# Kernel tuning notes

Hardware: AMD Instinct MI355X
Metric: run time of the kernel (lower is better)

## Reference

```python
import jax, jax.numpy as jnp
import numpy as np

EPS = 1e-12  # undefined global `eps` in the original source; standard tiny epsilon


def setup_inputs() -> dict:
    key = jax.random.key(0)
    k1, k2 = jax.random.split(key)
    B, C = 32768, 1000
    output = jax.random.normal(k1, (B, C), dtype=jnp.float32)
    multilabels = (jax.random.uniform(k2, (B, C)) < 0.05).astype(jnp.float32)
    multilabels = multilabels.at[:, 0].set(1.0)
    return {"output": output, "multilabels": multilabels}


def reference(output, multilabels):
    # Equivalent closed form of: for every nonempty subset g of true labels,
    #   loss(g) = -[ pseudo_y*log(o+eps) + (1-pseudo_y)*log(1-o+eps) ].sum()
    #           = base - sum_{j in g} gain_j,
    # with base = -sum_j log(1-o_j+eps) and gain_j = log(o_j+eps)-log(1-o_j+eps).
    # min over nonempty subsets = base - max nonempty-subset gain
    #   = base - (sum of positive gains over true labels, or the max single
    #      gain among true labels if all gains are negative).
    o = jax.nn.sigmoid(output)                      # [B, C]
    log_p = jnp.log(o + EPS)
    log_np = jnp.log(1.0 - o + EPS)
    base = -jnp.sum(log_np, axis=1)                 # [B]
    gain = log_p - log_np                           # [B, C]
    is_true = multilabels == 1.0                    # [B, C] bool (constant)
    pos = is_true & (gain > 0)
    pos_gain = jnp.sum(jnp.where(pos, gain, 0.0), axis=1)          # [B]
    any_pos = jnp.any(pos, axis=1)                                  # [B]
    best_single = jnp.max(jnp.where(is_true, gain, -jnp.inf), axis=1)  # [B]
    max_gain = jnp.where(any_pos, pos_gain, best_single)
    per_sample = base - max_gain                    # [B]
    return jnp.mean(per_sample)
```

## Files before the change

kernel.cpp:

```cpp
#include <hip/hip_runtime.h>
#include <math.h>


constexpr int B = 32768;
constexpr int C = 1000;
constexpr int BLOCKS = 2048;
constexpr int THREADS = 256;
constexpr int WAVES_PER_BLOCK = 4;

__device__ __forceinline__ void elem_update(float x, float m,
                                            float& base, float& pos, float& best) {
    float e  = __expf(-fabsf(x));
    float xp = fmaxf(x, 0.0f);
    base += xp + __logf(1.0f + e);
    pos  += m * xp;
    if (m != 0.0f) best = fmaxf(best, x);
}

__device__ __forceinline__ void vec_update(const float4& x, const float4& m,
                                           float& base, float& pos, float& best) {
    elem_update(x.x, m.x, base, pos, best);
    elem_update(x.y, m.y, base, pos, best);
    elem_update(x.z, m.z, base, pos, best);
    elem_update(x.w, m.w, base, pos, best);
}

__global__ __launch_bounds__(THREADS)
void row_loss_kernel(const float* __restrict__ X,
                     const float* __restrict__ M,
                     float* __restrict__ partial) {
    const int lane = threadIdx.x & 63;
    const int sub  = lane & 15;
    const int grp  = lane >> 4;
    const int wave_in_block = threadIdx.x >> 6;
    const int gwave = blockIdx.x * WAVES_PER_BLOCK + wave_in_block;
    const int row   = gwave * 4 + grp;

    const float4* x4 = reinterpret_cast<const float4*>(X + (size_t)row * C);
    const float4* m4 = reinterpret_cast<const float4*>(M + (size_t)row * C);

    float4 xA[4], mA[4], xB[4], mB[4];

    #pragma unroll
    for (int j = 0; j < 4; ++j) { int i = sub + 16*j;       xA[j] = x4[i]; mA[j] = m4[i]; }
    #pragma unroll
    for (int j = 0; j < 4; ++j) { int i = sub + 64 + 16*j;  xB[j] = x4[i]; mB[j] = m4[i]; }

    float base = 0.f, pos = 0.f, best = -INFINITY;

    #pragma unroll
    for (int j = 0; j < 4; ++j) vec_update(xA[j], mA[j], base, pos, best);

    #pragma unroll
    for (int j = 0; j < 4; ++j) { int i = sub + 128 + 16*j; xA[j] = x4[i]; mA[j] = m4[i]; }

    #pragma unroll
    for (int j = 0; j < 4; ++j) vec_update(xB[j], mB[j], base, pos, best);

    #pragma unroll
    for (int j = 0; j < 3; ++j) { int i = sub + 192 + 16*j; xB[j] = x4[i]; mB[j] = m4[i]; }
    if (sub < 10) { xB[3] = x4[sub + 240]; mB[3] = m4[sub + 240]; }
    else {
        xB[3] = make_float4(-1e30f, -1e30f, -1e30f, -1e30f);
        mB[3] = make_float4(0.f, 0.f, 0.f, 0.f);
    }

    #pragma unroll
    for (int j = 0; j < 4; ++j) vec_update(xA[j], mA[j], base, pos, best);
    #pragma unroll
    for (int j = 0; j < 4; ++j) vec_update(xB[j], mB[j], base, pos, best);

    #pragma unroll
    for (int off = 8; off > 0; off >>= 1) {
        base += __shfl_down(base, off, 16);
        pos  += __shfl_down(pos,  off, 16);
        best  = fmaxf(best, __shfl_down(best, off, 16));
    }

    float per = base - ((pos > 0.f) ? pos : best);
    float v = (sub == 0) ? per : 0.f;
    v += __shfl_down(v, 32, 64);
    v += __shfl_down(v, 16, 64);

    __shared__ float s[WAVES_PER_BLOCK];
    if (lane == 0) s[wave_in_block] = v;
    __syncthreads();
    if (threadIdx.x == 0) {
        float t = 0.0f;
        #pragma unroll
        for (int i = 0; i < WAVES_PER_BLOCK; ++i) t += s[i];
        partial[blockIdx.x] = t;
    }
}

__global__ __launch_bounds__(256)
void finalize_kernel(const float* __restrict__ partial, float* __restrict__ out) {
    double t = 0.0;
    for (int i = threadIdx.x; i < BLOCKS; i += 256) t += (double)partial[i];

    #pragma unroll
    for (int off = 32; off > 0; off >>= 1)
        t += __shfl_down(t, off, 64);

    __shared__ double s[4];
    const int lane = threadIdx.x & 63;
    const int w    = threadIdx.x >> 6;
    if (lane == 0) s[w] = t;
    __syncthreads();
    if (threadIdx.x == 0) {
        double r = s[0] + s[1] + s[2] + s[3];
        out[0] = (float)(r / (double)B);
    }
}

extern "C" void kernel_launch(void* const* d_in, const int* in_sizes, int n_in,
                              void* d_out, int out_size, void* d_ws, size_t ws_size,
                              hipStream_t stream) {
    const float* X  = (const float*)d_in[0];
    const float* M  = (const float*)d_in[1];
    float* out      = (float*)d_out;
    float* partial  = (float*)d_ws;

    row_loss_kernel<<<BLOCKS, THREADS, 0, stream>>>(X, M, partial);
    finalize_kernel<<<1, 256, 0, stream>>>(partial, out);
}
```

Measured before the change: 274.3 us.

## Map one row per 256-thread block with single float4 per thread

Replaces the 16-lanes-per-row mapping, where each lane loaded many float4s in a software-pipelined pattern, with one block per row in which each thread loads one float4 of logits and mask. Per-row reduction now uses a full-wave shuffle plus a shared-memory combine, and the finalize kernel sums 32768 per-row partials instead of 2048. This increases block count and parallelism per row, but leaves 6 of 256 threads idle, adds a barrier per row, and makes the single-block finalize read sixteen times more partials.

Result: slower. 293.0 us (+6.8%).

```diff
diff --git a/kernel.cpp b/kernel.cpp
--- a/kernel.cpp
+++ b/kernel.cpp
@@ -4,9 +4,8 @@
 
 constexpr int B = 32768;
 constexpr int C = 1000;
-constexpr int BLOCKS = 2048;
+constexpr int C4 = C / 4;
 constexpr int THREADS = 256;
-constexpr int WAVES_PER_BLOCK = 4;
 
 __device__ __forceinline__ void elem_update(float x, float m,
                                             float& base, float& pos, float& best) {
@@ -17,86 +16,50 @@
     if (m != 0.0f) best = fmaxf(best, x);
 }
 
-__device__ __forceinline__ void vec_update(const float4& x, const float4& m,
-                                           float& base, float& pos, float& best) {
-    elem_update(x.x, m.x, base, pos, best);
-    elem_update(x.y, m.y, base, pos, best);
-    elem_update(x.z, m.z, base, pos, best);
-    elem_update(x.w, m.w, base, pos, best);
-}
-
 __global__ __launch_bounds__(THREADS)
 void row_loss_kernel(const float* __restrict__ X,
                      const float* __restrict__ M,
                      float* __restrict__ partial) {
-    const int lane = threadIdx.x & 63;
-    const int sub  = lane & 15;
-    const int grp  = lane >> 4;
-    const int wave_in_block = threadIdx.x >> 6;
-    const int gwave = blockIdx.x * WAVES_PER_BLOCK + wave_in_block;
-    const int row   = gwave * 4 + grp;
-
-    const float4* x4 = reinterpret_cast<const float4*>(X + (size_t)row * C);
-    const float4* m4 = reinterpret_cast<const float4*>(M + (size_t)row * C);
-
-    float4 xA[4], mA[4], xB[4], mB[4];
-
-    #pragma unroll
-    for (int j = 0; j < 4; ++j) { int i = sub + 16*j;       xA[j] = x4[i]; mA[j] = m4[i]; }
-    #pragma unroll
-    for (int j = 0; j < 4; ++j) { int i = sub + 64 + 16*j;  xB[j] = x4[i]; mB[j] = m4[i]; }
+    const int row = blockIdx.x;
+    const int t   = threadIdx.x;
 
     float base = 0.f, pos = 0.f, best = -INFINITY;
 
-    #pragma unroll
-    for (int j = 0; j < 4; ++j) vec_update(xA[j], mA[j], base, pos, best);
-
-    #pragma unroll
-    for (int j = 0; j < 4; ++j) { int i = sub + 128 + 16*j; xA[j] = x4[i]; mA[j] = m4[i]; }
-
-    #pragma unroll
-    for (int j = 0; j < 4; ++j) vec_update(xB[j], mB[j], base, pos, best);
-
-    #pragma unroll
-    for (int j = 0; j < 3; ++j) { int i = sub + 192 + 16*j; xB[j] = x4[i]; mB[j] = m4[i]; }
-    if (sub < 10) { xB[3] = x4[sub + 240]; mB[3] = m4[sub + 240]; }
-    else {
-        xB[3] = make_float4(-1e30f, -1e30f, -1e30f, -1e30f);
-        mB[3] = make_float4(0.f, 0.f, 0.f, 0.f);
+    if (t < C4) {
+        const float4* x4 = reinterpret_cast<const float4*>(X + (size_t)row * C);
+        const float4* m4 = reinterpret_cast<const float4*>(M + (size_t)row * C);
+        float4 x = x4[t];
+        float4 m = m4[t];
+        elem_update(x.x, m.x, base, pos, best);
+        elem_update(x.y, m.y, base, pos, best);
+        elem_update(x.z, m.z, base, pos, best);
+        elem_update(x.w, m.w, base, pos, best);
     }
 
     #pragma unroll
-    for (int j = 0; j < 4; ++j) vec_update(xA[j], mA[j], base, pos, best);
-    #pragma unroll
-    for (int j = 0; j < 4; ++j) vec_update(xB[j], mB[j], base, pos, best);
-
-    #pragma unroll
-    for (int off = 8; off > 0; off >>= 1) {
-        base += __shfl_down(base, off, 16);
-        pos  += __shfl_down(pos,  off, 16);
-        best  = fmaxf(best, __shfl_down(best, off, 16));
+    for (int off = 32; off > 0; off >>= 1) {
+        base += __shfl_down(base, off, 64);
+        pos  += __shfl_down(pos,  off, 64);
+        best  = fmaxf(best, __shfl_down(best, off, 64));
     }
 
-    float per = base - ((pos > 0.f) ? pos : best);
-    float v = (sub == 0) ? per : 0.f;
-    v += __shfl_down(v, 32, 64);
-    v += __shfl_down(v, 16, 64);
-
-    __shared__ float s[WAVES_PER_BLOCK];
-    if (lane == 0) s[wave_in_block] = v;
+    __shared__ float sb[4], sp[4], ss[4];
+    const int w    = t >> 6;
+    const int lane = t & 63;
+    if (lane == 0) { sb[w] = base; sp[w] = pos; ss[w] = best; }
     __syncthreads();
-    if (threadIdx.x == 0) {
-        float t = 0.0f;
-        #pragma unroll
-        for (int i = 0; i < WAVES_PER_BLOCK; ++i) t += s[i];
-        partial[blockIdx.x] = t;
+    if (t == 0) {
+        float b = (sb[0] + sb[1]) + (sb[2] + sb[3]);
+        float p = (sp[0] + sp[1]) + (sp[2] + sp[3]);
+        float s = fmaxf(fmaxf(ss[0], ss[1]), fmaxf(ss[2], ss[3]));
+        partial[row] = b - ((p > 0.f) ? p : s);
     }
 }
 
 __global__ __launch_bounds__(256)
 void finalize_kernel(const float* __restrict__ partial, float* __restrict__ out) {
     double t = 0.0;
-    for (int i = threadIdx.x; i < BLOCKS; i += 256) t += (double)partial[i];
+    for (int i = threadIdx.x; i < B; i += 256) t += (double)partial[i];
 
     #pragma unroll
     for (int off = 32; off > 0; off >>= 1)
@@ -108,7 +71,7 @@
     if (lane == 0) s[w] = t;
     __syncthreads();
     if (threadIdx.x == 0) {
-        double r = s[0] + s[1] + s[2] + s[3];
+        double r = (s[0] + s[1]) + (s[2] + s[3]);
         out[0] = (float)(r / (double)B);
     }
 }
@@ -121,6 +84,6 @@
     float* out      = (float*)d_out;
     float* partial  = (float*)d_ws;
 
-    row_loss_kernel<<<BLOCKS, THREADS, 0, stream>>>(X, M, partial);
+    row_loss_kernel<<<B, THREADS, 0, stream>>>(X, M, partial);
     finalize_kernel<<<1, 256, 0, stream>>>(partial, out);
 }
```
